# Kernel optimization log

Measured on AMD Instinct MI355X. Metric: run time of the kernel, lower is better.

The kernel has to match this reference:

```python
import jax, jax.numpy as jnp
import numpy as np

B, S, H, DK, DV, DE = 2, 256, 8, 64, 64, 512
DT = H * DV
EPS = 1e-5

def _clin(xr, xi, W, b):
    # complex linear: x @ W + b with (re, im) parts; W: (2, d_in, d_out), b: (2, d_out)
    yr = xr @ W[0] - xi @ W[1] + b[0]
    yi = xr @ W[1] + xi @ W[0] + b[1]
    return yr, yi

def _emul(ar, ai, br, bi):
    # complex elementwise (Hadamard) multiply
    return ar * br - ai * bi, ar * bi + ai * br

def _forward(Z_q, Z_k, Z_v, t_measure_all, Wq, bq, Wk, bk, Wv, bv, Wp, bp,
             lambda_imag_v, lambda_real_v, lambda_omega_sqrt_v,
             lambda_gamma_sqrt_v, noise_floor, tau, eta_param):
    Bn = Z_q.shape[0]
    t = t_measure_all[0, :-1]
    t = t / (t[-1] - t[0])

    def heads(z, W, b, d):
        yr, yi = _clin(z[:, 0], z[:, 1], W, b)
        f = lambda a: a.reshape(Bn, S, H, d).swapaxes(-1, -2)  # (B,S,d,H)
        return f(yr), f(yi)

    Qr, Qi = heads(Z_q, Wq, bq, DK)
    Kr, Ki = heads(Z_k, Wk, bk, DK)
    Vr, Vi = heads(Z_v, Wv, bv, DV)

    # complex eigenvalues in conjugate pairs: (DV, H)
    lam_im = jnp.concatenate([lambda_imag_v, -lambda_imag_v], axis=1).T
    lam_re = jnp.broadcast_to(lambda_real_v[None, :], (DV, H))

    # forward/backward exponential kernels exp(+/- lambda t): (S, DV, H)
    phase = t[:, None, None] * lam_im[None]
    mag = jnp.exp(t[:, None, None] * lam_re[None])
    ef_r = mag * jnp.cos(phase); ef_i = mag * jnp.sin(phase)
    eb_r = jnp.cos(phase) / mag; eb_i = -jnp.sin(phase) / mag
    me_r, me_i = ef_r[0], ef_i[0]  # mat_exp

    # scalar covariance kernel per (i, j, head): process noise + measurement noise
    omega = lambda_omega_sqrt_v ** 2
    gamma = lambda_gamma_sqrt_v ** 2 + EPS
    dt = jnp.maximum(t[:, None] - t[None, :], 0.0)  # causal lags only
    den = 2.0 * lambda_real_v  # (H,)
    safe = jnp.where(jnp.abs(den) > 1e-6, den, 1.0)
    x = dt[:, :, None] * den
    g = jnp.where(jnp.abs(den) > 1e-6, jnp.expm1(x) / safe, dt[:, :, None])
    V_avg = omega * g + gamma * jnp.exp(x)  # (S,S,H)

    # factorized kernels: U_* = exp(-lambda t_j) * X_j ; propagator factor |exp(lambda t_i)|^2
    Uq_r, Uq_i = _emul(eb_r[None], eb_i[None], Qr, Qi)
    Uk_r, Uk_i = _emul(eb_r[None], eb_i[None], Kr, Ki)
    Uv_r, Uv_i = _emul(eb_r[None], eb_i[None], Vr, Vi)
    Vk2 = ef_r ** 2 + ef_i ** 2  # (S,DV,H)

    # precision-weighted residual norm |exp(lambda(t_i-t_j)) k_j - q_i|^2
    Uq2 = Uq_r ** 2 + Uq_i ** 2
    Uk2 = Uk_r ** 2 + Uk_i ** 2
    self_q = jnp.einsum('idh,bidh->bih', Vk2, Uq2)
    term_k = jnp.einsum('idh,bjdh->bijh', Vk2, Uk2)
    cross = (jnp.einsum('bidh,bjdh->bijh', Vk2[None] * Uq_r, Uk_r)
             + jnp.einsum('bidh,bjdh->bijh', Vk2[None] * Uq_i, Uk_i))
    R = term_k + self_q[:, :, None, :] - 2.0 * cross  # (B,S,S,H)

    base = (noise_floor ** 2 + EPS) * V_avg[None] + R
    scores = -(tau ** 2) * jnp.log(base)
    mask = jnp.tril(jnp.ones((S, S), bool))
    scores = jnp.where(mask[None, :, :, None], scores, -jnp.inf)
    attn = jax.nn.softmax(scores, axis=2)  # (B,S,S,H)

    # complex matmul with real-valued attention (imag part of Q_ij is zero)
    er = jnp.einsum('bijh,bjdh->bidh', attn, Uv_r)
    ei = jnp.einsum('bijh,bjdh->bidh', attn, Uv_i)
    est_r, est_i = _emul(ef_r[None], ef_i[None], er, ei)

    eta = jax.nn.sigmoid(eta_param)[0, 0]  # (1,DV,H)
    el_r = (1.0 - eta) * Vr + jax.nn.sigmoid(eta) * est_r
    el_i = (1.0 - eta) * Vi + jax.nn.sigmoid(eta) * est_i

    pr, pi = _emul(me_r[None, None], me_i[None, None], el_r, el_i)
    merge = lambda a: a.swapaxes(-1, -2).reshape(Bn, S, DT)
    o_r, o_i = _clin(merge(pr), merge(pi), Wp, bp)
    out = jnp.stack([o_r, o_i], axis=1)  # (B,2,S,DE)

    # all-pairs propagated estimates Z_ij = exp(lambda t_i) * U_v,j
    zr, zi = _emul(ef_r[None, :, None], ef_i[None, :, None],
                   Uv_r[:, None], Uv_i[:, None])  # (B,S,S,DV,H)
    zm = lambda a: a.swapaxes(-1, -2).reshape(Bn, S, S, DT)
    Z_ij = jnp.stack([zm(zr), zm(zi)], axis=1)  # (B,2,S,S,DT)

    est_latent = jnp.stack([el_r, el_i], axis=1)  # (B,2,S,DV,H)
    Q_ij = jnp.stack([attn, jnp.zeros_like(attn)], axis=1)
    epoch_lambdas = jnp.stack([lam_re, lam_im], 0).swapaxes(-1, -2).reshape(2, H * DV)[..., None]
    return est_latent, out, Q_ij, Z_ij, epoch_lambdas

def setup_inputs():
    key = jax.random.key(0)
    k = jax.random.split(key, 16)
    sc_in = 1.0 / np.sqrt(DE)
    sc_out = 1.0 / np.sqrt(DT)
    return {
        'Z_q': jax.random.normal(k[0], (B, 2, S, DE), jnp.float32),
        'Z_k': jax.random.normal(k[1], (B, 2, S, DE), jnp.float32),
        'Z_v': jax.random.normal(k[2], (B, 2, S, DE), jnp.float32),
        't_measure_all': jnp.arange(S + 1, dtype=jnp.float32)[None, :],
        'Wq': jax.random.normal(k[3], (2, DE, DT), jnp.float32) * sc_in,
        'bq': jax.random.normal(k[4], (2, DT), jnp.float32) * 0.01,
        'Wk': jax.random.normal(k[5], (2, DE, DT), jnp.float32) * sc_in,
        'bk': jax.random.normal(k[6], (2, DT), jnp.float32) * 0.01,
        'Wv': jax.random.normal(k[7], (2, DE, DT), jnp.float32) * sc_in,
        'bv': jax.random.normal(k[8], (2, DT), jnp.float32) * 0.01,
        'Wp': jax.random.normal(k[9], (2, DT, DE), jnp.float32) * sc_out,
        'bp': jax.random.normal(k[10], (2, DE), jnp.float32) * 0.01,
        'lambda_imag_v': jax.random.normal(k[11], (H, DV // 2), jnp.float32),
        'lambda_real_v': jax.random.normal(k[12], (H,), jnp.float32) * 0.5,
        'lambda_omega_sqrt_v': jax.random.normal(k[13], (H,), jnp.float32),
        'lambda_gamma_sqrt_v': jax.random.normal(k[14], (H,), jnp.float32),
        'noise_floor': jnp.ones((H,), jnp.float32),
        'tau': jnp.ones((H,), jnp.float32),
        'eta_param': jnp.zeros((1, 1, 1, DV, H), jnp.float32),
    }

def reference(Z_q, Z_k, Z_v, t_measure_all, Wq, bq, Wk, bk, Wv, bv, Wp, bp,
              lambda_imag_v, lambda_real_v, lambda_omega_sqrt_v,
              lambda_gamma_sqrt_v, noise_floor, tau, eta_param):
    return _forward(Z_q, Z_k, Z_v, t_measure_all, Wq, bq, Wk, bk, Wv, bv, Wp, bp,
                    lambda_imag_v, lambda_real_v, lambda_omega_sqrt_v,
                    lambda_gamma_sqrt_v, noise_floor, tau, eta_param)
```

## Files before the change

### kernel.cpp

```cpp
#include <hip/hip_runtime.h>
#include <hip/hip_bf16.h>
#include <math.h>

constexpr int kB  = 2;
constexpr int kS  = 256;
constexpr int kH  = 8;
constexpr float kEPS = 1e-5f;

constexpr int OFF_EST = 0;
constexpr int OFF_OUT = 524288;
constexpr int OFF_QIJ = 1048576;
constexpr int OFF_ZIJ = 3145728;
constexpr int OFF_EPO = 137363456;

constexpr int WS_EFR = 0;
constexpr int WS_EFI = 131072;
constexpr int WS_EBR = 262144;
constexpr int WS_EBI = 393216;
constexpr int WS_UQR = 524288;
constexpr int WS_UQI = 786432;
constexpr int WS_UKR = 1048576;
constexpr int WS_UKI = 1310720;
constexpr int WS_UVR = 1572864;
constexpr int WS_UVI = 1835008;
constexpr int WS_VR  = 2097152;
constexpr int WS_VI  = 2359296;
constexpr int WS_BF  = 3145728;

constexpr int A2Q = 0;
constexpr int A2K = 524288;
constexpr int A2V = 1048576;
constexpr int B2R0 = 1572864;

typedef __attribute__((ext_vector_type(8))) short bf16x8;
typedef __attribute__((ext_vector_type(4))) float f32x4;
typedef __attribute__((ext_vector_type(8))) unsigned short u16x8;
typedef __attribute__((ext_vector_type(4))) unsigned short u16x4;

__device__ __forceinline__ float sigm(float x) { return 1.f / (1.f + expf(-x)); }
__device__ __forceinline__ unsigned short f2b(float f) {
    __hip_bfloat16 h = __float2bfloat16(f);
    return *reinterpret_cast<unsigned short*>(&h);
}

__global__ __launch_bounds__(256) void k_precompute(
    const float* __restrict__ tall, const float* __restrict__ Lim,
    const float* __restrict__ Lre,
    float* __restrict__ efr, float* __restrict__ efi,
    float* __restrict__ ebr, float* __restrict__ ebi,
    float* __restrict__ epo)
{
    int idx = blockIdx.x * 256 + threadIdx.x;
    int s = idx >> 9;
    int c = idx & 511;
    int h = c >> 6;
    int d = c & 63;
    float li = (d < 32) ? Lim[h * 32 + d] : -Lim[h * 32 + d - 32];
    float lr = Lre[h];
    float t  = tall[s] / (tall[kS - 1] - tall[0]);
    float ph  = t * li;
    float mag = expf(t * lr);
    float cp  = cosf(ph);
    float sp  = sinf(ph);
    efr[idx] = mag * cp;
    efi[idx] = mag * sp;
    ebr[idx] = cp / mag;
    ebi[idx] = -sp / mag;
    if (s == 0) {
        epo[c]       = lr;
        epo[512 + c] = li;
    }
}

__global__ __launch_bounds__(256) void k_convA(
    const float* __restrict__ zq, const float* __restrict__ zk,
    const float* __restrict__ zv, __hip_bfloat16* __restrict__ bfbase)
{
    int idx = blockIdx.x * 256 + threadIdx.x;
    int tz  = idx >> 16;
    int rem = idx & 65535;
    int m   = rem >> 7;
    int k0  = (rem & 127) * 8;
    const float* src = (tz == 0) ? zq : (tz == 1) ? zk : zv;
    int b = m >> 8, s = m & 255;
    int c = (k0 >= 512) ? 1 : 0;
    int e = k0 - c * 512;
    const float* p = src + ((b * 2 + c) * 256 + s) * 512 + e;
    float4 v0 = *(const float4*)p;
    float4 v1 = *(const float4*)(p + 4);
    u16x8 o;
    o[0] = f2b(v0.x); o[1] = f2b(v0.y); o[2] = f2b(v0.z); o[3] = f2b(v0.w);
    o[4] = f2b(v1.x); o[5] = f2b(v1.y); o[6] = f2b(v1.z); o[7] = f2b(v1.w);
    __hip_bfloat16* dst = bfbase + ((tz == 0) ? A2Q : (tz == 1) ? A2K : A2V)
                          + m * 1024 + k0;
    *(u16x8*)dst = o;
}

__global__ __launch_bounds__(256) void k_convW(
    const float* __restrict__ wq, const float* __restrict__ wk,
    const float* __restrict__ wv, const float* __restrict__ wp,
    __hip_bfloat16* __restrict__ bfbase)
{
    __shared__ float s0[64][65];
    __shared__ float s1[64][65];
    const int z = blockIdx.z;
    const float* W  = (z == 0) ? wq : (z == 1) ? wk : (z == 2) ? wv : wp;
    const float* W0 = W;
    const float* W1 = W + 262144;
    const int k0 = blockIdx.x * 64;
    const int n0 = blockIdx.y * 64;
    const int kp = k0 & 511;
    const bool hf = (k0 >= 512);
    const int t = threadIdx.x;
    const int r = t >> 2;
    const int q = t & 3;
#pragma unroll
    for (int c = 0; c < 4; ++c) {
        int col = q * 16 + c * 4;
        *(float4*)&s0[r][col] = *(const float4*)&W0[(kp + r) * 512 + n0 + col];
        *(float4*)&s1[r][col] = *(const float4*)&W1[(kp + r) * 512 + n0 + col];
    }
    __syncthreads();
    u16x8 r0, r1, i0, i1;
#pragma unroll
    for (int u = 0; u < 8; ++u) {
        int kl = q * 16 + u;
        float w0 = s0[kl][r], w1 = s1[kl][r];
        r0[u] = f2b(hf ? -w1 : w0);
        i0[u] = f2b(hf ?  w0 : w1);
    }
#pragma unroll
    for (int u = 0; u < 8; ++u) {
        int kl = q * 16 + 8 + u;
        float w0 = s0[kl][r], w1 = s1[kl][r];
        r1[u] = f2b(hf ? -w1 : w0);
        i1[u] = f2b(hf ?  w0 : w1);
    }
    __hip_bfloat16* pr = bfbase + B2R0 + z * 1048576
                         + (size_t)(n0 + r) * 1024 + k0 + q * 16;
    __hip_bfloat16* pi = pr + 524288;
    *(u16x8*)pr       = r0;
    *(u16x8*)(pr + 8) = r1;
    *(u16x8*)pi       = i0;
    *(u16x8*)(pi + 8) = i1;
}

template<bool IS_P>
__global__ __launch_bounds__(256) void k_cmfma(
    const __hip_bfloat16* __restrict__ bfbase,
    const __hip_bfloat16* __restrict__ a2p,
    const float* __restrict__ bq, const float* __restrict__ bk,
    const float* __restrict__ bv, const float* __restrict__ bp,
    const float* __restrict__ ebr, const float* __restrict__ ebi,
    float* __restrict__ uqr, float* __restrict__ uqi,
    float* __restrict__ ukr, float* __restrict__ uki,
    float* __restrict__ uvr, float* __restrict__ uvi,
    float* __restrict__ vr,  float* __restrict__ vi,
    float* __restrict__ outp)
{
    __shared__ __align__(16) char sm[24576];
    char* sA  = sm;
    char* sBr = sm + 8192;
    char* sBi = sm + 16384;

    const int mode = IS_P ? 3 : (int)blockIdx.z;
    const __hip_bfloat16* A2 = IS_P ? a2p
        : bfbase + ((mode == 0) ? A2Q : (mode == 1) ? A2K : A2V);
    const __hip_bfloat16* Br = bfbase + B2R0 + mode * 1048576;
    const __hip_bfloat16* Bi = Br + 524288;
    const float* bias = IS_P ? bp : ((mode == 0) ? bq : (mode == 1) ? bk : bv);

    const int tid = threadIdx.x;
    const int m0 = blockIdx.y * 64;
    const int n0 = blockIdx.x * 64;
    const int lane = tid & 63;
    const int wv2 = tid >> 6;
    const int wr = wv2 >> 1, wc = wv2 & 1;
    const int lx = lane & 15, lhi = lane >> 4;

    const int srow  = tid >> 2;
    const int sslot = (tid & 3) * 32;

    const char* gA  = (const char*)(A2 + (size_t)(m0 + srow) * 1024);
    const char* gBr = (const char*)(Br + (size_t)(n0 + srow) * 1024);
    const char* gBi = (const char*)(Bi + (size_t)(n0 + srow) * 1024);
    const int swz = (srow & 7) << 4;
    char* dA  = sA  + srow * 128;
    char* dBr = sBr + srow * 128;
    char* dBi = sBi + srow * 128;

    f32x4 accR[2][2] = {};
    f32x4 accI[2][2] = {};

    int rowA[2], rowB[2];
    rowA[0] = wr * 32 + lx;  rowA[1] = rowA[0] + 16;
    rowB[0] = wc * 32 + lx;  rowB[1] = rowB[0] + 16;

    for (int kt = 0; kt < 16; ++kt) {
        const int kb = kt * 128;
        {
            float4 a0 = *(const float4*)(gA  + kb + sslot);
            float4 a1 = *(const float4*)(gA  + kb + sslot + 16);
            float4 b0 = *(const float4*)(gBr + kb + sslot);
            float4 b1 = *(const float4*)(gBr + kb + sslot + 16);
            float4 c0 = *(const float4*)(gBi + kb + sslot);
            float4 c1 = *(const float4*)(gBi + kb + sslot + 16);
            *(float4*)(dA  + ( sslot       ^ swz)) = a0;
            *(float4*)(dA  + ((sslot + 16) ^ swz)) = a1;
            *(float4*)(dBr + ( sslot       ^ swz)) = b0;
            *(float4*)(dBr + ((sslot + 16) ^ swz)) = b1;
            *(float4*)(dBi + ( sslot       ^ swz)) = c0;
            *(float4*)(dBi + ((sslot + 16) ^ swz)) = c1;
        }
        __syncthreads();
#pragma unroll
        for (int kk = 0; kk < 2; ++kk) {
            const int kbyte = kk * 64 + lhi * 16;
            bf16x8 af[2], brf[2], bif[2];
#pragma unroll
            for (int x = 0; x < 2; ++x) {
                int ra = rowA[x];
                af[x]  = *(const bf16x8*)(sA  + ra * 128 + (kbyte ^ ((ra & 7) << 4)));
                int rb = rowB[x];
                brf[x] = *(const bf16x8*)(sBr + rb * 128 + (kbyte ^ ((rb & 7) << 4)));
                bif[x] = *(const bf16x8*)(sBi + rb * 128 + (kbyte ^ ((rb & 7) << 4)));
            }
#pragma unroll
            for (int a = 0; a < 2; ++a)
#pragma unroll
                for (int bb = 0; bb < 2; ++bb) {
                    accR[a][bb] = __builtin_amdgcn_mfma_f32_16x16x32_bf16(
                        af[a], brf[bb], accR[a][bb], 0, 0, 0);
                    accI[a][bb] = __builtin_amdgcn_mfma_f32_16x16x32_bf16(
                        af[a], bif[bb], accI[a][bb], 0, 0, 0);
                }
        }
        __syncthreads();
    }

#pragma unroll
    for (int a = 0; a < 2; ++a) {
#pragma unroll
        for (int bb = 0; bb < 2; ++bb) {
#pragma unroll
            for (int j = 0; j < 4; ++j) {
                int m = m0 + wr * 32 + a * 16 + lhi * 4 + j;
                int n = n0 + wc * 32 + bb * 16 + lx;
                float yr = accR[a][bb][j] + bias[n];
                float yi = accI[a][bb][j] + bias[512 + n];
                int b = m >> 8, s = m & 255;
                if (IS_P) {
                    int rowo = m * 512 + b * 131072;
                    outp[rowo + n] = yr;
                    outp[rowo + 131072 + n] = yi;
                } else {
                    int h = n >> 6, d = n & 63;
                    float er_ = ebr[s * 512 + n], ei_ = ebi[s * 512 + n];
                    float ur = er_ * yr - ei_ * yi;
                    float ui = er_ * yi + ei_ * yr;
                    if (mode == 0) {
                        int idx = ((b * 8 + h) * 256 + s) * 64 + d;
                        uqr[idx] = ur; uqi[idx] = ui;
                    } else if (mode == 1) {
                        int idx = ((b * 8 + h) * 64 + d) * 256 + s;
                        ukr[idx] = ur; uki[idx] = ui;
                    } else {
                        int idx = ((b * 8 + h) * 256 + s) * 64 + d;
                        uvr[idx] = ur; uvi[idx] = ui;
                        int vidx = (b * 256 + s) * 512 + d * 8 + h;
                        vr[vidx] = yr; vi[vidx] = yi;
                    }
                }
            }
        }
    }
}

__global__ __launch_bounds__(256) void k_zij_attn(
    const float* __restrict__ efr, const float* __restrict__ efi,
    const float* __restrict__ uvr, const float* __restrict__ uvi,
    float* __restrict__ zout,
    const float* __restrict__ uqr, const float* __restrict__ uqi,
    const float* __restrict__ ukr, const float* __restrict__ uki,
    const float* __restrict__ tall,
    const float* __restrict__ Lre, const float* __restrict__ Lom,
    const float* __restrict__ Lga, const float* __restrict__ NF,
    const float* __restrict__ TAU,
    float* __restrict__ qij,
    const float* __restrict__ vr,  const float* __restrict__ vi,
    const float* __restrict__ ETA,
    float* __restrict__ out_est, __hip_bfloat16* __restrict__ a2p)
{
    __shared__ __align__(16) char smem[66688];
    float (*sP)[257] = (float(*)[257])smem;
    float (*sKr)[32] = (float(*)[32])(smem + 32896);
    float (*sKi)[32] = (float(*)[32])(smem + 41088);
    float (*sQr)[68] = (float(*)[68])(smem + 49280);
    float (*sQi)[68] = (float(*)[68])(smem + 57984);
    float (*sVr)[64] = (float(*)[64])(smem + 32896);
    float (*sVi)[64] = (float(*)[64])(smem + 41088);

    const int bid = blockIdx.x;
    const int tid = threadIdx.x;

    if (bid >= 128) {
        const int z  = bid - 128;
        const int j0 = (z & 63) * 4;
        const int i  = (z >> 6) & 255;
        const int b  = z >> 14;
#pragma unroll
        for (int half = 0; half < 2; half++) {
            int dt = half * 256 + tid;
            float fr = efr[i * 512 + dt];
            float fi = efi[i * 512 + dt];
            int h = dt >> 6, d = dt & 63;
            const float* ur = uvr + ((b * 8 + h) * 256) * 64 + d;
            const float* ui = uvi + ((b * 8 + h) * 256) * 64 + d;
#pragma unroll
            for (int jj = 0; jj < 4; jj++) {
                int j = j0 + jj;
                float vr_ = ur[j * 64];
                float vi_ = ui[j * 64];
                float zr = fr * vr_ - fi * vi_;
                float zi = fr * vi_ + fi * vr_;
                int idx0 = (b * 2) * 33554432 + i * 131072 + j * 512 + dt;
                __builtin_nontemporal_store(zr, &zout[idx0]);
                __builtin_nontemporal_store(zi, &zout[idx0 + 33554432]);
            }
        }
        return;
    }

    const int it = bid & 7;
    const int h  = (bid >> 3) & 7;
    const int b  = bid >> 6;
    const int i0 = it * 32;
    const int ti = tid >> 3;
    const int tj = tid & 7;
    const int i  = i0 + ti;

    {
        const float* qsr = uqr + ((b * 8 + h) * 256 + i) * 64;
        const float* qsi = uqi + ((b * 8 + h) * 256 + i) * 64;
        *(float4*)&sQr[ti][tj * 4]      = *(const float4*)&qsr[tj * 4];
        *(float4*)&sQr[ti][32 + tj * 4] = *(const float4*)&qsr[32 + tj * 4];
        *(float4*)&sQi[ti][tj * 4]      = *(const float4*)&qsi[tj * 4];
        *(float4*)&sQi[ti][32 + tj * 4] = *(const float4*)&qsi[32 + tj * 4];
    }

    const float lre  = Lre[h];
    const float om   = Lom[h] * Lom[h];
    const float ga   = Lga[h] * Lga[h] + kEPS;
    const float nf2  = NF[h] * NF[h] + kEPS;
    const float tau2 = TAU[h] * TAU[h];
    const float den  = 2.f * lre;
    const float invT = 1.f / (tall[kS - 1] - tall[0]);
    const float t_i  = tall[i] * invT;
    const float m2i  = expf(2.f * t_i * lre);
    const bool  denok = fabsf(den) > 1e-6f;

    const int kr2 = tid >> 2;
    const int kq2 = tid & 3;

    for (int jt = 0; jt <= it; ++jt) {
        const int j0 = jt * 32;
        __syncthreads();
        {
            const float* ksrc_r = ukr + ((b * 8 + h) * 64 + kr2) * 256 + j0;
            const float* ksrc_i = uki + ((b * 8 + h) * 64 + kr2) * 256 + j0;
            *(float4*)&sKr[kr2][kq2 * 4]      = *(const float4*)&ksrc_r[kq2 * 4];
            *(float4*)&sKr[kr2][16 + kq2 * 4] = *(const float4*)&ksrc_r[16 + kq2 * 4];
            *(float4*)&sKi[kr2][kq2 * 4]      = *(const float4*)&ksrc_i[kq2 * 4];
            *(float4*)&sKi[kr2][16 + kq2 * 4] = *(const float4*)&ksrc_i[16 + kq2 * 4];
        }
        __syncthreads();

        float acc[4] = {0.f, 0.f, 0.f, 0.f};
#pragma unroll 16
        for (int d = 0; d < 64; d++) {
            float qr = sQr[ti][d];
            float qi = sQi[ti][d];
            float4 kr = *(float4*)&sKr[d][tj * 4];
            float4 ki = *(float4*)&sKi[d][tj * 4];
#define DSTEP(c, KRC, KIC)                                    \
            { float dr = qr - KRC; float di = qi - KIC;       \
              acc[c] = fmaf(dr, dr, acc[c]);                  \
              acc[c] = fmaf(di, di, acc[c]); }
            DSTEP(0, kr.x, ki.x)
            DSTEP(1, kr.y, ki.y)
            DSTEP(2, kr.z, ki.z)
            DSTEP(3, kr.w, ki.w)
#undef DSTEP
        }

#pragma unroll
        for (int c = 0; c < 4; c++) {
            int j = j0 + tj * 4 + c;
            if (j <= i) {
                float t_j = tall[j] * invT;
                float dtt = fmaxf(t_i - t_j, 0.f);
                float x = dtt * den;
                float g = denok ? (expm1f(x) / den) : dtt;
                float Vv = om * g + ga * expf(x);
                float base = nf2 * Vv + m2i * acc[c];
                sP[ti][j] = -tau2 * logf(base);
            }
        }
    }
    __syncthreads();

    float mx = -1e30f;
    for (int j = tj; j <= i; j += 8) mx = fmaxf(mx, sP[ti][j]);
#pragma unroll
    for (int m = 1; m < 8; m <<= 1) mx = fmaxf(mx, __shfl_xor(mx, m));
    float sum = 0.f;
    for (int j = tj; j <= i; j += 8) {
        float e = expf(sP[ti][j] - mx);
        sP[ti][j] = e;
        sum += e;
    }
#pragma unroll
    for (int m = 1; m < 8; m <<= 1) sum += __shfl_xor(sum, m);
    const float inv = 1.f / sum;

    float* srow   = qij + ((b * 512 + i) * 256) * 8 + h;
    float* qi_out = qij + ((b * 512 + 256 + i) * 256) * 8 + h;
    const int jfill = i0 + 32;
    for (int j = tj; j < 256; j += 8) {
        float p = 0.f;
        if (j <= i) p = sP[ti][j] * inv;
        if (j < jfill) sP[ti][j] = p;
        srow[j * 8]   = p;
        qi_out[j * 8] = 0.f;
    }
    __syncthreads();

    const int dl = tid & 7;
    float accR[8] = {0.f}, accI[8] = {0.f};

    for (int jt = 0; jt <= it; jt++) {
        const int j0 = jt * 32;
        {
            const float* sr = uvr + ((b * 8 + h) * 256 + j0 + ti) * 64;
            const float* si = uvi + ((b * 8 + h) * 256 + j0 + ti) * 64;
            *(float4*)&sVr[ti][dl * 4]      = *(const float4*)&sr[dl * 4];
            *(float4*)&sVr[ti][32 + dl * 4] = *(const float4*)&sr[32 + dl * 4];
            *(float4*)&sVi[ti][dl * 4]      = *(const float4*)&si[dl * 4];
            *(float4*)&sVi[ti][32 + dl * 4] = *(const float4*)&si[32 + dl * 4];
        }
        __syncthreads();

#pragma unroll 8
        for (int jj = 0; jj < 32; jj++) {
            float a = sP[ti][j0 + jj];
            float4 v0 = *(float4*)&sVr[jj][dl * 8];
            float4 v1 = *(float4*)&sVr[jj][dl * 8 + 4];
            float4 w0 = *(float4*)&sVi[jj][dl * 8];
            float4 w1 = *(float4*)&sVi[jj][dl * 8 + 4];
            float vv[8] = {v0.x, v0.y, v0.z, v0.w, v1.x, v1.y, v1.z, v1.w};
            float ww[8] = {w0.x, w0.y, w0.z, w0.w, w1.x, w1.y, w1.z, w1.w};
#pragma unroll
            for (int c = 0; c < 8; c++) {
                accR[c] = fmaf(a, vv[c], accR[c]);
                accI[c] = fmaf(a, ww[c], accI[c]);
            }
        }
        __syncthreads();
    }

    const int cb = h * 64 + dl * 8;
    f32x4 fr0 = *(const f32x4*)&efr[i * 512 + cb];
    f32x4 fr1 = *(const f32x4*)&efr[i * 512 + cb + 4];
    f32x4 fi0 = *(const f32x4*)&efi[i * 512 + cb];
    f32x4 fi1 = *(const f32x4*)&efi[i * 512 + cb + 4];
    f32x4 mr0 = *(const f32x4*)&efr[cb];
    f32x4 mr1 = *(const f32x4*)&efr[cb + 4];
    f32x4 mi0 = *(const f32x4*)&efi[cb];
    f32x4 mi1 = *(const f32x4*)&efi[cb + 4];

    u16x8 o_r, o_i;
#pragma unroll
    for (int c = 0; c < 8; c++) {
        float fr = (c < 4) ? fr0[c] : fr1[c - 4];
        float fi = (c < 4) ? fi0[c] : fi1[c - 4];
        float mr = (c < 4) ? mr0[c] : mr1[c - 4];
        float mi = (c < 4) ? mi0[c] : mi1[c - 4];
        int p = dl * 64 + c * 8 + h;
        float estr = fr * accR[c] - fi * accI[c];
        float esti = fr * accI[c] + fi * accR[c];
        float et = sigm(ETA[p]);
        float w1 = 1.f - et;
        float w2 = sigm(et);
        float vr_ = vr[(b * 256 + i) * 512 + p];
        float vi_ = vi[(b * 256 + i) * 512 + p];
        float elr = w1 * vr_ + w2 * estr;
        float eli = w1 * vi_ + w2 * esti;
        out_est[((b * 2 + 0) * 256 + i) * 512 + p] = elr;
        out_est[((b * 2 + 1) * 256 + i) * 512 + p] = eli;
        o_r[c] = f2b(mr * elr - mi * eli);
        o_i[c] = f2b(mr * eli + mi * elr);
    }
    __hip_bfloat16* ap = a2p + (b * 256 + i) * 1024 + cb;
    *(u16x8*)ap         = o_r;
    *(u16x8*)(ap + 512) = o_i;
}

extern "C" void kernel_launch(void* const* d_in, const int* in_sizes, int n_in,
                              void* d_out, int out_size, void* d_ws, size_t ws_size,
                              hipStream_t stream)
{
    const float* Zq   = (const float*)d_in[0];
    const float* Zk   = (const float*)d_in[1];
    const float* Zv   = (const float*)d_in[2];
    const float* tall = (const float*)d_in[3];
    const float* Wq   = (const float*)d_in[4];
    const float* bq   = (const float*)d_in[5];
    const float* Wk   = (const float*)d_in[6];
    const float* bk   = (const float*)d_in[7];
    const float* Wv   = (const float*)d_in[8];
    const float* bv   = (const float*)d_in[9];
    const float* Wp   = (const float*)d_in[10];
    const float* bp   = (const float*)d_in[11];
    const float* Lim  = (const float*)d_in[12];
    const float* Lre  = (const float*)d_in[13];
    const float* Lom  = (const float*)d_in[14];
    const float* Lga  = (const float*)d_in[15];
    const float* NF   = (const float*)d_in[16];
    const float* TAU  = (const float*)d_in[17];
    const float* ETA  = (const float*)d_in[18];

    float* out = (float*)d_out;
    float* ws  = (float*)d_ws;

    float* efr = ws + WS_EFR; float* efi = ws + WS_EFI;
    float* ebr = ws + WS_EBR; float* ebi = ws + WS_EBI;
    float* uqr = ws + WS_UQR; float* uqi = ws + WS_UQI;
    float* ukr = ws + WS_UKR; float* uki = ws + WS_UKI;
    float* uvr = ws + WS_UVR; float* uvi = ws + WS_UVI;
    float* vr  = ws + WS_VR;  float* vi  = ws + WS_VI;
    __hip_bfloat16* bfbase = (__hip_bfloat16*)(ws + WS_BF);
    __hip_bfloat16* a2p    = (__hip_bfloat16*)(ws + WS_EBR);

    k_precompute<<<512, 256, 0, stream>>>(tall, Lim, Lre, efr, efi, ebr, ebi,
                                          out + OFF_EPO);
    k_convA<<<768, 256, 0, stream>>>(Zq, Zk, Zv, bfbase);
    k_convW<<<dim3(16, 8, 4), 256, 0, stream>>>(Wq, Wk, Wv, Wp, bfbase);

    k_cmfma<false><<<dim3(8, 8, 3), 256, 0, stream>>>(
        bfbase, nullptr, bq, bk, bv, bp, ebr, ebi,
        uqr, uqi, ukr, uki, uvr, uvi, vr, vi, nullptr);

    k_zij_attn<<<32896, 256, 0, stream>>>(
        efr, efi, uvr, uvi, out + OFF_ZIJ,
        uqr, uqi, ukr, uki, tall, Lre, Lom, Lga, NF, TAU,
        out + OFF_QIJ, vr, vi, ETA, out + OFF_EST, a2p);

    k_cmfma<true><<<dim3(8, 8, 1), 256, 0, stream>>>(
        bfbase, a2p, bq, bk, bv, bp, ebr, ebi,
        nullptr, nullptr, nullptr, nullptr, nullptr, nullptr, nullptr, nullptr,
        out + OFF_OUT);
}
```

Measured before the change: 145.4 us.

## Merge prep kernels and overlap output projection with second-batch Zij stores

The three small preprocessing kernels (exponential tables, activation bf16 conversion, weight conversion) are merged into one launch that dispatches on block index. The large Zij store work is split by batch. Batch 0 stays in the attention kernel, while batch 1 moves into a new kernel that also runs the final complex output projection GEMM in its first 64 blocks. This removes launch gaps and lets the tail-end projection GEMM overlap with bandwidth-bound Zij stores, at the cost of more branchy kernels and uneven block work.

```diff
diff --git a/kernel.cpp b/kernel.cpp
--- a/kernel.cpp
+++ b/kernel.cpp
@@ -43,132 +43,127 @@
     return *reinterpret_cast<unsigned short*>(&h);
 }
 
-__global__ __launch_bounds__(256) void k_precompute(
+__global__ __launch_bounds__(256) void k_prep(
     const float* __restrict__ tall, const float* __restrict__ Lim,
     const float* __restrict__ Lre,
+    const float* __restrict__ zq, const float* __restrict__ zk,
+    const float* __restrict__ zv,
+    const float* __restrict__ wq, const float* __restrict__ wk,
+    const float* __restrict__ wv, const float* __restrict__ wp,
     float* __restrict__ efr, float* __restrict__ efi,
     float* __restrict__ ebr, float* __restrict__ ebi,
-    float* __restrict__ epo)
-{
-    int idx = blockIdx.x * 256 + threadIdx.x;
-    int s = idx >> 9;
-    int c = idx & 511;
-    int h = c >> 6;
-    int d = c & 63;
-    float li = (d < 32) ? Lim[h * 32 + d] : -Lim[h * 32 + d - 32];
-    float lr = Lre[h];
-    float t  = tall[s] / (tall[kS - 1] - tall[0]);
-    float ph  = t * li;
-    float mag = expf(t * lr);
-    float cp  = cosf(ph);
-    float sp  = sinf(ph);
-    efr[idx] = mag * cp;
-    efi[idx] = mag * sp;
-    ebr[idx] = cp / mag;
-    ebi[idx] = -sp / mag;
-    if (s == 0) {
-        epo[c]       = lr;
-        epo[512 + c] = li;
-    }
-}
-
-__global__ __launch_bounds__(256) void k_convA(
-    const float* __restrict__ zq, const float* __restrict__ zk,
-    const float* __restrict__ zv, __hip_bfloat16* __restrict__ bfbase)
-{
-    int idx = blockIdx.x * 256 + threadIdx.x;
-    int tz  = idx >> 16;
-    int rem = idx & 65535;
-    int m   = rem >> 7;
-    int k0  = (rem & 127) * 8;
-    const float* src = (tz == 0) ? zq : (tz == 1) ? zk : zv;
-    int b = m >> 8, s = m & 255;
-    int c = (k0 >= 512) ? 1 : 0;
-    int e = k0 - c * 512;
-    const float* p = src + ((b * 2 + c) * 256 + s) * 512 + e;
-    float4 v0 = *(const float4*)p;
-    float4 v1 = *(const float4*)(p + 4);
-    u16x8 o;
-    o[0] = f2b(v0.x); o[1] = f2b(v0.y); o[2] = f2b(v0.z); o[3] = f2b(v0.w);
-    o[4] = f2b(v1.x); o[5] = f2b(v1.y); o[6] = f2b(v1.z); o[7] = f2b(v1.w);
-    __hip_bfloat16* dst = bfbase + ((tz == 0) ? A2Q : (tz == 1) ? A2K : A2V)
-                          + m * 1024 + k0;
-    *(u16x8*)dst = o;
-}
-
-__global__ __launch_bounds__(256) void k_convW(
-    const float* __restrict__ wq, const float* __restrict__ wk,
-    const float* __restrict__ wv, const float* __restrict__ wp,
-    __hip_bfloat16* __restrict__ bfbase)
+    float* __restrict__ epo, __hip_bfloat16* __restrict__ bfbase)
 {
     __shared__ float s0[64][65];
     __shared__ float s1[64][65];
-    const int z = blockIdx.z;
-    const float* W  = (z == 0) ? wq : (z == 1) ? wk : (z == 2) ? wv : wp;
-    const float* W0 = W;
-    const float* W1 = W + 262144;
-    const int k0 = blockIdx.x * 64;
-    const int n0 = blockIdx.y * 64;
-    const int kp = k0 & 511;
-    const bool hf = (k0 >= 512);
-    const int t = threadIdx.x;
-    const int r = t >> 2;
-    const int q = t & 3;
-#pragma unroll
-    for (int c = 0; c < 4; ++c) {
-        int col = q * 16 + c * 4;
-        *(float4*)&s0[r][col] = *(const float4*)&W0[(kp + r) * 512 + n0 + col];
-        *(float4*)&s1[r][col] = *(const float4*)&W1[(kp + r) * 512 + n0 + col];
-    }
-    __syncthreads();
-    u16x8 r0, r1, i0, i1;
-#pragma unroll
-    for (int u = 0; u < 8; ++u) {
-        int kl = q * 16 + u;
-        float w0 = s0[kl][r], w1 = s1[kl][r];
-        r0[u] = f2b(hf ? -w1 : w0);
-        i0[u] = f2b(hf ?  w0 : w1);
-    }
-#pragma unroll
-    for (int u = 0; u < 8; ++u) {
-        int kl = q * 16 + 8 + u;
-        float w0 = s0[kl][r], w1 = s1[kl][r];
-        r1[u] = f2b(hf ? -w1 : w0);
-        i1[u] = f2b(hf ?  w0 : w1);
-    }
-    __hip_bfloat16* pr = bfbase + B2R0 + z * 1048576
-                         + (size_t)(n0 + r) * 1024 + k0 + q * 16;
-    __hip_bfloat16* pi = pr + 524288;
-    *(u16x8*)pr       = r0;
-    *(u16x8*)(pr + 8) = r1;
-    *(u16x8*)pi       = i0;
-    *(u16x8*)(pi + 8) = i1;
+    const int bid = blockIdx.x;
+    const int tid = threadIdx.x;
+
+    if (bid < 512) {
+        int idx = bid * 256 + tid;
+        int s = idx >> 9;
+        int c = idx & 511;
+        int h = c >> 6;
+        int d = c & 63;
+        float li = (d < 32) ? Lim[h * 32 + d] : -Lim[h * 32 + d - 32];
+        float lr = Lre[h];
+        float t  = tall[s] / (tall[kS - 1] - tall[0]);
+        float ph  = t * li;
+        float mag = expf(t * lr);
+        float cp  = cosf(ph);
+        float sp  = sinf(ph);
+        efr[idx] = mag * cp;
+        efi[idx] = mag * sp;
+        ebr[idx] = cp / mag;
+        ebi[idx] = -sp / mag;
+        if (s == 0) {
+            epo[c]       = lr;
+            epo[512 + c] = li;
+        }
+    } else if (bid < 1280) {
+        int idx = (bid - 512) * 256 + tid;
+        int tz  = idx >> 16;
+        int rem = idx & 65535;
+        int m   = rem >> 7;
+        int k0  = (rem & 127) * 8;
+        const float* src = (tz == 0) ? zq : (tz == 1) ? zk : zv;
+        int b = m >> 8, s = m & 255;
+        int c = (k0 >= 512) ? 1 : 0;
+        int e = k0 - c * 512;
+        const float* p = src + ((b * 2 + c) * 256 + s) * 512 + e;
+        float4 v0 = *(const float4*)p;
+        float4 v1 = *(const float4*)(p + 4);
+        u16x8 o;
+        o[0] = f2b(v0.x); o[1] = f2b(v0.y); o[2] = f2b(v0.z); o[3] = f2b(v0.w);
+        o[4] = f2b(v1.x); o[5] = f2b(v1.y); o[6] = f2b(v1.z); o[7] = f2b(v1.w);
+        __hip_bfloat16* dst = bfbase + ((tz == 0) ? A2Q : (tz == 1) ? A2K : A2V)
+                              + m * 1024 + k0;
+        *(u16x8*)dst = o;
+    } else {
+        int wid = bid - 1280;
+        int z = wid >> 7;
+        int r2 = wid & 127;
+        int k0 = (r2 & 15) * 64;
+        int n0 = (r2 >> 4) * 64;
+        const float* W  = (z == 0) ? wq : (z == 1) ? wk : (z == 2) ? wv : wp;
+        const float* W0 = W;
+        const float* W1 = W + 262144;
+        const int kp = k0 & 511;
+        const bool hf = (k0 >= 512);
+        const int r = tid >> 2;
+        const int q = tid & 3;
+#pragma unroll
+        for (int c = 0; c < 4; ++c) {
+            int col = q * 16 + c * 4;
+            *(float4*)&s0[r][col] = *(const float4*)&W0[(kp + r) * 512 + n0 + col];
+            *(float4*)&s1[r][col] = *(const float4*)&W1[(kp + r) * 512 + n0 + col];
+        }
+        __syncthreads();
+        u16x8 r0, r1, i0, i1;
+#pragma unroll
+        for (int u = 0; u < 8; ++u) {
+            int kl = q * 16 + u;
+            float w0 = s0[kl][r], w1 = s1[kl][r];
+            r0[u] = f2b(hf ? -w1 : w0);
+            i0[u] = f2b(hf ?  w0 : w1);
+        }
+#pragma unroll
+        for (int u = 0; u < 8; ++u) {
+            int kl = q * 16 + 8 + u;
+            float w0 = s0[kl][r], w1 = s1[kl][r];
+            r1[u] = f2b(hf ? -w1 : w0);
+            i1[u] = f2b(hf ?  w0 : w1);
+        }
+        __hip_bfloat16* pr = bfbase + B2R0 + z * 1048576
+                             + (size_t)(n0 + r) * 1024 + k0 + q * 16;
+        __hip_bfloat16* pi = pr + 524288;
+        *(u16x8*)pr       = r0;
+        *(u16x8*)(pr + 8) = r1;
+        *(u16x8*)pi       = i0;
+        *(u16x8*)(pi + 8) = i1;
+    }
 }
 
-template<bool IS_P>
-__global__ __launch_bounds__(256) void k_cmfma(
+__global__ __launch_bounds__(256) void k_cmfma_qkv(
     const __hip_bfloat16* __restrict__ bfbase,
-    const __hip_bfloat16* __restrict__ a2p,
     const float* __restrict__ bq, const float* __restrict__ bk,
-    const float* __restrict__ bv, const float* __restrict__ bp,
+    const float* __restrict__ bv,
     const float* __restrict__ ebr, const float* __restrict__ ebi,
     float* __restrict__ uqr, float* __restrict__ uqi,
     float* __restrict__ ukr, float* __restrict__ uki,
     float* __restrict__ uvr, float* __restrict__ uvi,
-    float* __restrict__ vr,  float* __restrict__ vi,
-    float* __restrict__ outp)
+    float* __restrict__ vr,  float* __restrict__ vi)
 {
     __shared__ __align__(16) char sm[24576];
     char* sA  = sm;
     char* sBr = sm + 8192;
     char* sBi = sm + 16384;
 
-    const int mode = IS_P ? 3 : (int)blockIdx.z;
-    const __hip_bfloat16* A2 = IS_P ? a2p
-        : bfbase + ((mode == 0) ? A2Q : (mode == 1) ? A2K : A2V);
+    const int mode = (int)blockIdx.z;
+    const __hip_bfloat16* A2 = bfbase + ((mode == 0) ? A2Q : (mode == 1) ? A2K : A2V);
     const __hip_bfloat16* Br = bfbase + B2R0 + mode * 1048576;
     const __hip_bfloat16* Bi = Br + 524288;
-    const float* bias = IS_P ? bp : ((mode == 0) ? bq : (mode == 1) ? bk : bv);
+    const float* bias = (mode == 0) ? bq : (mode == 1) ? bk : bv;
 
     const int tid = threadIdx.x;
     const int m0 = blockIdx.y * 64;
@@ -249,27 +244,21 @@
                 float yr = accR[a][bb][j] + bias[n];
                 float yi = accI[a][bb][j] + bias[512 + n];
                 int b = m >> 8, s = m & 255;
-                if (IS_P) {
-                    int rowo = m * 512 + b * 131072;
-                    outp[rowo + n] = yr;
-                    outp[rowo + 131072 + n] = yi;
+                int h = n >> 6, d = n & 63;
+                float er_ = ebr[s * 512 + n], ei_ = ebi[s * 512 + n];
+                float ur = er_ * yr - ei_ * yi;
+                float ui = er_ * yi + ei_ * yr;
+                if (mode == 0) {
+                    int idx = ((b * 8 + h) * 256 + s) * 64 + d;
+                    uqr[idx] = ur; uqi[idx] = ui;
+                } else if (mode == 1) {
+                    int idx = ((b * 8 + h) * 64 + d) * 256 + s;
+                    ukr[idx] = ur; uki[idx] = ui;
                 } else {
-                    int h = n >> 6, d = n & 63;
-                    float er_ = ebr[s * 512 + n], ei_ = ebi[s * 512 + n];
-                    float ur = er_ * yr - ei_ * yi;
-                    float ui = er_ * yi + ei_ * yr;
-                    if (mode == 0) {
-                        int idx = ((b * 8 + h) * 256 + s) * 64 + d;
-                        uqr[idx] = ur; uqi[idx] = ui;
-                    } else if (mode == 1) {
-                        int idx = ((b * 8 + h) * 64 + d) * 256 + s;
-                        ukr[idx] = ur; uki[idx] = ui;
-                    } else {
-                        int idx = ((b * 8 + h) * 256 + s) * 64 + d;
-                        uvr[idx] = ur; uvi[idx] = ui;
-                        int vidx = (b * 256 + s) * 512 + d * 8 + h;
-                        vr[vidx] = yr; vi[vidx] = yi;
-                    }
+                    int idx = ((b * 8 + h) * 256 + s) * 64 + d;
+                    uvr[idx] = ur; uvi[idx] = ui;
+                    int vidx = (b * 256 + s) * 512 + d * 8 + h;
+                    vr[vidx] = yr; vi[vidx] = yi;
                 }
             }
         }
@@ -306,8 +295,8 @@
     if (bid >= 128) {
         const int z  = bid - 128;
         const int j0 = (z & 63) * 4;
-        const int i  = (z >> 6) & 255;
-        const int b  = z >> 14;
+        const int i  = z >> 6;
+        const int b  = 0;
 #pragma unroll
         for (int half = 0; half < 2; half++) {
             int dt = half * 256 + tid;
@@ -503,6 +492,142 @@
     __hip_bfloat16* ap = a2p + (b * 256 + i) * 1024 + cb;
     *(u16x8*)ap         = o_r;
     *(u16x8*)(ap + 512) = o_i;
+}
+
+__global__ __launch_bounds__(256) void k_zij_proj(
+    const float* __restrict__ efr, const float* __restrict__ efi,
+    const float* __restrict__ uvr, const float* __restrict__ uvi,
+    float* __restrict__ zout,
+    const __hip_bfloat16* __restrict__ bfbase,
+    const __hip_bfloat16* __restrict__ a2p,
+    const float* __restrict__ bp,
+    float* __restrict__ outp)
+{
+    __shared__ __align__(16) char sm[24576];
+
+    const int bid = blockIdx.x;
+    const int tid = threadIdx.x;
+
+    if (bid >= 64) {
+        const int z  = bid - 64;
+        const int j0 = (z & 63) * 4;
+        const int i  = z >> 6;
+        const int b  = 1;
+#pragma unroll
+        for (int half = 0; half < 2; half++) {
+            int dt = half * 256 + tid;
+            float fr = efr[i * 512 + dt];
+            float fi = efi[i * 512 + dt];
+            int h = dt >> 6, d = dt & 63;
+            const float* ur = uvr + ((b * 8 + h) * 256) * 64 + d;
+            const float* ui = uvi + ((b * 8 + h) * 256) * 64 + d;
+#pragma unroll
+            for (int jj = 0; jj < 4; jj++) {
+                int j = j0 + jj;
+                float vr_ = ur[j * 64];
+                float vi_ = ui[j * 64];
+                float zr = fr * vr_ - fi * vi_;
+                float zi = fr * vi_ + fi * vr_;
+                int idx0 = (b * 2) * 33554432 + i * 131072 + j * 512 + dt;
+                __builtin_nontemporal_store(zr, &zout[idx0]);
+                __builtin_nontemporal_store(zi, &zout[idx0 + 33554432]);
+            }
+        }
+        return;
+    }
+
+    char* sA  = sm;
+    char* sBr = sm + 8192;
+    char* sBi = sm + 16384;
+
+    const __hip_bfloat16* A2 = a2p;
+    const __hip_bfloat16* Br = bfbase + B2R0 + 3 * 1048576;
+    const __hip_bfloat16* Bi = Br + 524288;
+
+    const int m0 = (bid >> 3) * 64;
+    const int n0 = (bid & 7) * 64;
+    const int lane = tid & 63;
+    const int wv2 = tid >> 6;
+    const int wr = wv2 >> 1, wc = wv2 & 1;
+    const int lx = lane & 15, lhi = lane >> 4;
+
+    const int srow  = tid >> 2;
+    const int sslot = (tid & 3) * 32;
+
+    const char* gA  = (const char*)(A2 + (size_t)(m0 + srow) * 1024);
+    const char* gBr = (const char*)(Br + (size_t)(n0 + srow) * 1024);
+    const char* gBi = (const char*)(Bi + (size_t)(n0 + srow) * 1024);
+    const int swz = (srow & 7) << 4;
+    char* dA  = sA  + srow * 128;
+    char* dBr = sBr + srow * 128;
+    char* dBi = sBi + srow * 128;
+
+    f32x4 accR[2][2] = {};
+    f32x4 accI[2][2] = {};
+
+    int rowA[2], rowB[2];
+    rowA[0] = wr * 32 + lx;  rowA[1] = rowA[0] + 16;
+    rowB[0] = wc * 32 + lx;  rowB[1] = rowB[0] + 16;
+
+    for (int kt = 0; kt < 16; ++kt) {
+        const int kb = kt * 128;
+        {
+            float4 a0 = *(const float4*)(gA  + kb + sslot);
+            float4 a1 = *(const float4*)(gA  + kb + sslot + 16);
+            float4 b0 = *(const float4*)(gBr + kb + sslot);
+            float4 b1 = *(const float4*)(gBr + kb + sslot + 16);
+            float4 c0 = *(const float4*)(gBi + kb + sslot);
+            float4 c1 = *(const float4*)(gBi + kb + sslot + 16);
+            *(float4*)(dA  + ( sslot       ^ swz)) = a0;
+            *(float4*)(dA  + ((sslot + 16) ^ swz)) = a1;
+            *(float4*)(dBr + ( sslot       ^ swz)) = b0;
+            *(float4*)(dBr + ((sslot + 16) ^ swz)) = b1;
+            *(float4*)(dBi + ( sslot       ^ swz)) = c0;
+            *(float4*)(dBi + ((sslot + 16) ^ swz)) = c1;
+        }
+        __syncthreads();
+#pragma unroll
+        for (int kk = 0; kk < 2; ++kk) {
+            const int kbyte = kk * 64 + lhi * 16;
+            bf16x8 af[2], brf[2], bif[2];
+#pragma unroll
+            for (int x = 0; x < 2; ++x) {
+                int ra = rowA[x];
+                af[x]  = *(const bf16x8*)(sA  + ra * 128 + (kbyte ^ ((ra & 7) << 4)));
+                int rb = rowB[x];
+                brf[x] = *(const bf16x8*)(sBr + rb * 128 + (kbyte ^ ((rb & 7) << 4)));
+                bif[x] = *(const bf16x8*)(sBi + rb * 128 + (kbyte ^ ((rb & 7) << 4)));
+            }
+#pragma unroll
+            for (int a = 0; a < 2; ++a)
+#pragma unroll
+                for (int bb = 0; bb < 2; ++bb) {
+                    accR[a][bb] = __builtin_amdgcn_mfma_f32_16x16x32_bf16(
+                        af[a], brf[bb], accR[a][bb], 0, 0, 0);
+                    accI[a][bb] = __builtin_amdgcn_mfma_f32_16x16x32_bf16(
+                        af[a], bif[bb], accI[a][bb], 0, 0, 0);
+                }
+        }
+        __syncthreads();
+    }
+
+#pragma unroll
+    for (int a = 0; a < 2; ++a) {
+#pragma unroll
+        for (int bb = 0; bb < 2; ++bb) {
+#pragma unroll
+            for (int j = 0; j < 4; ++j) {
+                int m = m0 + wr * 32 + a * 16 + lhi * 4 + j;
+                int n = n0 + wc * 32 + bb * 16 + lx;
+                float yr = accR[a][bb][j] + bp[n];
+                float yi = accI[a][bb][j] + bp[512 + n];
+                int b = m >> 8;
+                int rowo = m * 512 + b * 131072;
+                outp[rowo + n] = yr;
+                outp[rowo + 131072 + n] = yi;
+            }
+        }
+    }
 }
 
 extern "C" void kernel_launch(void* const* d_in, const int* in_sizes, int n_in,
@@ -541,22 +666,21 @@
     __hip_bfloat16* bfbase = (__hip_bfloat16*)(ws + WS_BF);
     __hip_bfloat16* a2p    = (__hip_bfloat16*)(ws + WS_EBR);
 
-    k_precompute<<<512, 256, 0, stream>>>(tall, Lim, Lre, efr, efi, ebr, ebi,
-                                          out + OFF_EPO);
-    k_convA<<<768, 256, 0, stream>>>(Zq, Zk, Zv, bfbase);
-    k_convW<<<dim3(16, 8, 4), 256, 0, stream>>>(Wq, Wk, Wv, Wp, bfbase);
-
-    k_cmfma<false><<<dim3(8, 8, 3), 256, 0, stream>>>(
-        bfbase, nullptr, bq, bk, bv, bp, ebr, ebi,
-        uqr, uqi, ukr, uki, uvr, uvi, vr, vi, nullptr);
-
-    k_zij_attn<<<32896, 256, 0, stream>>>(
+    k_prep<<<1792, 256, 0, stream>>>(tall, Lim, Lre, Zq, Zk, Zv,
+                                     Wq, Wk, Wv, Wp,
+                                     efr, efi, ebr, ebi,
+                                     out + OFF_EPO, bfbase);
+
+    k_cmfma_qkv<<<dim3(8, 8, 3), 256, 0, stream>>>(
+        bfbase, bq, bk, bv, ebr, ebi,
+        uqr, uqi, ukr, uki, uvr, uvi, vr, vi);
+
+    k_zij_attn<<<16512, 256, 0, stream>>>(
         efr, efi, uvr, uvi, out + OFF_ZIJ,
         uqr, uqi, ukr, uki, tall, Lre, Lom, Lga, NF, TAU,
         out + OFF_QIJ, vr, vi, ETA, out + OFF_EST, a2p);
 
-    k_cmfma<true><<<dim3(8, 8, 1), 256, 0, stream>>>(
-        bfbase, a2p, bq, bk, bv, bp, ebr, ebi,
-        nullptr, nullptr, nullptr, nullptr, nullptr, nullptr, nullptr, nullptr,
-        out + OFF_OUT);
+    k_zij_proj<<<16448, 256, 0, stream>>>(
+        efr, efi, uvr, uvi, out + OFF_ZIJ,
+        bfbase, a2p, bp, out + OFF_OUT);
 }
```

New measurement: 155.3 us. +6.8%, slower.
